# Performance work log

Measured on AMD Instinct MI355X. Metric: run time of the kernel, lower is better.

## Reference

```python
import jax, jax.numpy as jnp
import numpy as np

B, TQ, TV, D, UNITS = 16, 2048, 2048, 1024, 1024

def setup_inputs() -> dict:
    key = jax.random.key(0)
    k1, k2, k3 = jax.random.split(key, 3)
    query = jax.random.normal(k1, (B, TQ, UNITS), dtype=jnp.float32)
    values = jax.random.normal(k2, (B, TV, D), dtype=jnp.float32)
    # Glorot-ish scale for the Dense kernel
    W_kernel = jax.random.normal(k3, (D, UNITS), dtype=jnp.float32) * (1.0 / np.sqrt(D))
    W_bias = jnp.zeros((UNITS,), dtype=jnp.float32)
    return {"query": query, "values": values, "W_kernel": W_kernel, "W_bias": W_bias}

def reference(query, values, W_kernel, W_bias):
    # keys = Dense(values): [B, Tv, units]
    keys = jnp.einsum('bvd,du->bvu', values, W_kernel) + W_bias
    # score = query @ keys^T: [B, Tq, Tv]
    score = jnp.einsum('bqu,bvu->bqv', query, keys)
    alignment = jax.nn.softmax(score, axis=-1)
    # context = alignment @ values: [B, Tq, d_v]
    context = jnp.einsum('bqv,bvd->bqd', alignment, values)
    return (context, alignment)
```

## Files before the change

kernel.cpp:

```cpp
#include <hip/hip_runtime.h>
#include <hip/hip_bf16.h>


#define B_  16
#define TQ_ 2048
#define TV_ 2048
#define D_  1024
#define U_  1024

typedef __attribute__((ext_vector_type(8))) short bf16x8;
typedef __attribute__((ext_vector_type(4))) float f32x4;

__device__ __forceinline__ short f2bf(float x) {
    union { float f; unsigned u; } v; v.f = x;
    unsigned r = v.u + 0x7fffu + ((v.u >> 16) & 1u);
    return (short)(r >> 16);
}
__device__ __forceinline__ float bf2f(short h) {
    union { unsigned u; float f; } v;
    v.u = ((unsigned)(unsigned short)h) << 16;
    return v.f;
}

__device__ __forceinline__ void gld16(const short* g, short* l) {
    __builtin_amdgcn_global_load_lds(
        (const __attribute__((address_space(1))) void*)g,
        (__attribute__((address_space(3))) void*)l, 16, 0, 0);
}

#define MFMA_QUAD(MB, NB)                                                       \
    __builtin_amdgcn_s_setprio(1);                                              \
    _Pragma("unroll")                                                           \
    for (int mf = 0; mf < 4; ++mf)                                              \
        _Pragma("unroll")                                                       \
        for (int nf = 0; nf < 2; ++nf)                                          \
            _Pragma("unroll")                                                   \
            for (int ks = 0; ks < 2; ++ks)                                      \
                acc[(MB) + mf][(NB) + nf] =                                     \
                    __builtin_amdgcn_mfma_f32_16x16x32_bf16(                    \
                        afr[mf][ks], bfr[(NB) + nf][ks],                        \
                        acc[(MB) + mf][(NB) + nf], 0, 0, 0);                    \
    __builtin_amdgcn_s_setprio(0);

template<int NPLANES, int SPLIT_OUT, int KT>
__global__ __launch_bounds__(512, 2) void gemm8(
    const short* __restrict__ Ahi, const short* __restrict__ Alo,
    const short* __restrict__ Bhi, const short* __restrict__ Blo,
    float* __restrict__ C, short* __restrict__ Chi, short* __restrict__ Clo,
    int lda, int ldb, int ldc, size_t sAz, size_t sBz, size_t sCz)
{
    constexpr int NT = NPLANES * KT;
    __shared__ short sA[2][16384];
    __shared__ short sB[2][16384];

    const int tid  = threadIdx.x;
    const int lane = tid & 63, wid = tid >> 6;
    const int wm = (wid >> 2) << 7;
    const int wn = (wid & 3) << 6;
    const int l15 = lane & 15, l4 = lane >> 4, l7 = lane & 7;
    const int sr   = tid >> 3;
    const int colS = ((tid & 7) ^ (sr & 7)) << 3;
    const int wvB  = wid << 9;

    const size_t z    = blockIdx.z;
    const size_t row0 = (size_t)blockIdx.y << 8;
    const size_t col0 = (size_t)blockIdx.x << 8;
    const short* Abh = Ahi + z * sAz + row0 * (size_t)lda;
    const short* Abl = (NPLANES == 3) ? Alo + z * sAz + row0 * (size_t)lda : nullptr;
    const short* Bbh = Bhi + z * sBz + col0 * (size_t)ldb;
    const short* Bbl = (NPLANES == 3) ? Blo + z * sBz + col0 * (size_t)ldb : nullptr;

    auto aSrc = [&](int t) -> const short* {
        const int p = t / KT;
        const short* base = (NPLANES == 3 && p == 2) ? Abl : Abh;
        return base + ((t - p * KT) << 6);
    };
    auto bSrc = [&](int t) -> const short* {
        const int p = t / KT;
        const short* base = (NPLANES == 3 && p == 1) ? Bbl : Bbh;
        return base + ((t - p * KT) << 6);
    };
    auto stageA = [&](int t, int h) {
        const short* g = aSrc(t) + (size_t)((h << 7) + sr) * lda + colS;
        short* l = &sA[t & 1][(h << 13) + wvB];
        gld16(g, l);
        gld16(g + (size_t)(lda << 6), l + 4096);
    };
    auto stageB = [&](int t, int h) {
        const short* g = bSrc(t) + (size_t)((h << 7) + sr) * ldb + colS;
        short* l = &sB[t & 1][(h << 13) + wvB];
        gld16(g, l);
        gld16(g + (size_t)(ldb << 6), l + 4096);
    };

    f32x4 acc[8][4];
    #pragma unroll
    for (int i = 0; i < 8; ++i)
        #pragma unroll
        for (int j = 0; j < 4; ++j)
            acc[i][j] = (f32x4){0.f, 0.f, 0.f, 0.f};

    stageB(0, 0); stageB(0, 1); stageA(0, 0); stageA(0, 1);
    stageB(1, 0); stageB(1, 1); stageA(1, 0);
    asm volatile("s_waitcnt vmcnt(6)" ::: "memory");
    __builtin_amdgcn_s_barrier();

    #pragma unroll 1
    for (int t = 0; t < NT; ++t) {
        const short* sAb = sA[t & 1];
        const short* sBb = sB[t & 1];
        bf16x8 afr[4][2], bfr[4][2];

        #pragma unroll
        for (int nf = 0; nf < 4; ++nf)
            #pragma unroll
            for (int ks = 0; ks < 2; ++ks)
                bfr[nf][ks] = *(const bf16x8*)&sBb[((wn + (nf << 4) + l15) << 6)
                                + ((((ks << 2) | l4) ^ l7) << 3)];
        #pragma unroll
        for (int mf = 0; mf < 4; ++mf)
            #pragma unroll
            for (int ks = 0; ks < 2; ++ks)
                afr[mf][ks] = *(const bf16x8*)&sAb[((wm + (mf << 4) + l15) << 6)
                                + ((((ks << 2) | l4) ^ l7) << 3)];
        if (t + 1 < NT) stageA(t + 1, 1);
        __builtin_amdgcn_s_barrier();
        asm volatile("s_waitcnt lgkmcnt(0)" ::: "memory");
        __builtin_amdgcn_sched_barrier(0);
        MFMA_QUAD(0, 0)
        __builtin_amdgcn_s_barrier();

        if (t + 2 < NT) stageB(t + 2, 0);
        __builtin_amdgcn_s_barrier();
        MFMA_QUAD(0, 2)
        __builtin_amdgcn_s_barrier();

        #pragma unroll
        for (int mf = 0; mf < 4; ++mf)
            #pragma unroll
            for (int ks = 0; ks < 2; ++ks)
                afr[mf][ks] = *(const bf16x8*)&sAb[((wm + 64 + (mf << 4) + l15) << 6)
                                + ((((ks << 2) | l4) ^ l7) << 3)];
        if (t + 2 < NT) stageB(t + 2, 1);
        __builtin_amdgcn_s_barrier();
        asm volatile("s_waitcnt lgkmcnt(0)" ::: "memory");
        __builtin_amdgcn_sched_barrier(0);
        MFMA_QUAD(4, 2)
        __builtin_amdgcn_s_barrier();

        if (t + 2 < NT) stageA(t + 2, 0);
        __builtin_amdgcn_s_barrier();
        MFMA_QUAD(4, 0)
        if (t < NT - 2)       asm volatile("s_waitcnt vmcnt(6)" ::: "memory");
        else if (t == NT - 2) asm volatile("s_waitcnt vmcnt(0)" ::: "memory");
        __builtin_amdgcn_s_barrier();
    }

    if (SPLIT_OUT) {
        #pragma unroll
        for (int mf = 0; mf < 8; ++mf)
            #pragma unroll
            for (int nf = 0; nf < 4; ++nf)
                #pragma unroll
                for (int r = 0; r < 4; ++r) {
                    const float x = acc[mf][nf][r];
                    const short h = f2bf(x);
                    const short lo = f2bf(x - bf2f(h));
                    const size_t idx = (row0 + wm + (mf << 4) + (l4 << 2) + r) * (size_t)ldc
                                       + col0 + wn + (nf << 4) + l15;
                    Chi[idx] = h;
                    Clo[idx] = lo;
                }
    } else {
        float* Cb = C + z * sCz;
        #pragma unroll
        for (int mf = 0; mf < 8; ++mf)
            #pragma unroll
            for (int nf = 0; nf < 4; ++nf)
                #pragma unroll
                for (int r = 0; r < 4; ++r)
                    Cb[(row0 + wm + (mf << 4) + (l4 << 2) + r) * (size_t)ldc
                       + col0 + wn + (nf << 4) + l15] = acc[mf][nf][r];
    }
}

__global__ __launch_bounds__(256, 2) void gemm_ctx(
    const float* __restrict__ A, const short* __restrict__ Bt, float* __restrict__ C,
    int lda, int ldb, int ldc, int K, size_t sA, size_t sB, size_t sC)
{
    __shared__ short sA16[128 * 32], sB16[128 * 32];
    const int tid = threadIdx.x;
    const int lane = tid & 63, wave = tid >> 6;
    const int wm = (wave >> 1) << 6, wn = (wave & 1) << 6;
    const int l15 = lane & 15, l4 = lane >> 4;
    const int lr = lane >> 2, lc = (lane & 3) << 3;
    const size_t row0 = (size_t)blockIdx.y << 7, col0 = (size_t)blockIdx.x << 7;
    const float* Ab = A + (size_t)blockIdx.z * sA + row0 * (size_t)lda;
    const short* Bb = Bt + (size_t)blockIdx.z * sB + col0 * (size_t)ldb;

    f32x4 acc[4][4];
    for (int i = 0; i < 4; ++i)
        for (int j = 0; j < 4; ++j)
            acc[i][j] = (f32x4){0.f, 0.f, 0.f, 0.f};

    for (int kt = 0; kt < K; kt += 32) {
        __syncthreads();
        for (int r = 0; r < 4; ++r) {
            const int flat = (r << 8) + tid;
            const int row = flat >> 3, c = (flat & 7) << 2;
            const float4 va = *(const float4*)(Ab + (size_t)row * lda + kt + c);
            short4 h;
            h.x = f2bf(va.x); h.y = f2bf(va.y); h.z = f2bf(va.z); h.w = f2bf(va.w);
            *(short4*)&sA16[(row << 5) + c] = h;
        }
        for (int t = 0; t < 2; ++t) {
            const int rbase = (wave << 5) + (t << 4);
            gld16(Bb + (size_t)(rbase + lr) * ldb + kt + lc, &sB16[rbase << 5]);
        }
        __syncthreads();
        const int ko = l4 << 3;
        bf16x8 ah[4], bh[4];
        for (int i = 0; i < 4; ++i) {
            ah[i] = *(const bf16x8*)&sA16[((wm + (i << 4) + l15) << 5) + ko];
            bh[i] = *(const bf16x8*)&sB16[((wn + (i << 4) + l15) << 5) + ko];
        }
        for (int i = 0; i < 4; ++i)
            for (int j = 0; j < 4; ++j)
                acc[i][j] = __builtin_amdgcn_mfma_f32_16x16x32_bf16(ah[i], bh[j], acc[i][j], 0, 0, 0);
    }

    float* Cb = C + (size_t)blockIdx.z * sC;
    for (int i = 0; i < 4; ++i)
        for (int j = 0; j < 4; ++j)
            for (int r = 0; r < 4; ++r)
                Cb[(row0 + wm + (i << 4) + (l4 << 2) + r) * (size_t)ldc
                   + col0 + wn + (j << 4) + l15] = acc[i][j][r];
}

__global__ __launch_bounds__(256) void split_f32(
    const float* __restrict__ X, short* __restrict__ hi, short* __restrict__ lo)
{
    const size_t i = ((size_t)blockIdx.x * 256 + threadIdx.x) << 2;
    const float4 v = *(const float4*)(X + i);
    short4 h, l;
    h.x = f2bf(v.x); l.x = f2bf(v.x - bf2f(h.x));
    h.y = f2bf(v.y); l.y = f2bf(v.y - bf2f(h.y));
    h.z = f2bf(v.z); l.z = f2bf(v.z - bf2f(h.z));
    h.w = f2bf(v.w); l.w = f2bf(v.w - bf2f(h.w));
    *(short4*)(hi + i) = h;
    *(short4*)(lo + i) = l;
}

__global__ __launch_bounds__(256) void split_values(
    const float* __restrict__ V, short* __restrict__ Vhi,
    short* __restrict__ Vlo, short* __restrict__ Vt)
{
    __shared__ float tile[32][33];
    const int b = blockIdx.z;
    const int d0 = blockIdx.x << 5, v0 = blockIdx.y << 5;
    const float* Vb = V + (size_t)b * TV_ * D_;
    const size_t pb = (size_t)b * TV_ * D_;
    short* Vtb = Vt + (size_t)b * D_ * TV_;
    const int tx = threadIdx.x, ty = threadIdx.y;
    for (int k = 0; k < 4; ++k) {
        const int v = v0 + ty + (k << 3);
        const float x = Vb[(size_t)v * D_ + d0 + tx];
        tile[ty + (k << 3)][tx] = x;
        const short h = f2bf(x);
        Vhi[pb + (size_t)v * D_ + d0 + tx] = h;
        Vlo[pb + (size_t)v * D_ + d0 + tx] = f2bf(x - bf2f(h));
    }
    __syncthreads();
    for (int k = 0; k < 4; ++k)
        Vtb[(size_t)(d0 + ty + (k << 3)) * TV_ + v0 + tx] = f2bf(tile[tx][ty + (k << 3)]);
}

__global__ __launch_bounds__(256) void softmax_rows(
    float* __restrict__ S, short* __restrict__ A16)
{
    float* p = S + (size_t)blockIdx.x * TV_;
    const int t = threadIdx.x;
    const int lane = t & 63, wave = t >> 6;
    float4 a = *(const float4*)(p + (t << 2));
    float4 b = *(const float4*)(p + 1024 + (t << 2));
    float m = fmaxf(fmaxf(fmaxf(a.x, a.y), fmaxf(a.z, a.w)),
                    fmaxf(fmaxf(b.x, b.y), fmaxf(b.z, b.w)));
    for (int off = 32; off; off >>= 1) m = fmaxf(m, __shfl_xor(m, off, 64));
    __shared__ float redm[4], reds[4];
    if (lane == 0) redm[wave] = m;
    __syncthreads();
    m = fmaxf(fmaxf(redm[0], redm[1]), fmaxf(redm[2], redm[3]));
    a.x = __expf(a.x - m); a.y = __expf(a.y - m);
    a.z = __expf(a.z - m); a.w = __expf(a.w - m);
    b.x = __expf(b.x - m); b.y = __expf(b.y - m);
    b.z = __expf(b.z - m); b.w = __expf(b.w - m);
    float s = a.x + a.y + a.z + a.w + b.x + b.y + b.z + b.w;
    for (int off = 32; off; off >>= 1) s += __shfl_xor(s, off, 64);
    if (lane == 0) reds[wave] = s;
    __syncthreads();
    s = reds[0] + reds[1] + reds[2] + reds[3];
    const float inv = 1.0f / s;
    a.x *= inv; a.y *= inv; a.z *= inv; a.w *= inv;
    b.x *= inv; b.y *= inv; b.z *= inv; b.w *= inv;
    *(float4*)(p + (t << 2)) = a;
    *(float4*)(p + 1024 + (t << 2)) = b;
    if (A16) {
        short* q = A16 + (size_t)blockIdx.x * TV_;
        short4 ha, hb;
        ha.x = f2bf(a.x); ha.y = f2bf(a.y); ha.z = f2bf(a.z); ha.w = f2bf(a.w);
        hb.x = f2bf(b.x); hb.y = f2bf(b.y); hb.z = f2bf(b.z); hb.w = f2bf(b.w);
        *(short4*)(q + (t << 2)) = ha;
        *(short4*)(q + 1024 + (t << 2)) = hb;
    }
}

extern "C" void kernel_launch(void* const* d_in, const int* in_sizes, int n_in,
                              void* d_out, int out_size, void* d_ws, size_t ws_size,
                              hipStream_t stream)
{
    const float* query  = (const float*)d_in[0];
    const float* values = (const float*)d_in[1];
    const float* Wk     = (const float*)d_in[2];

    const size_t NQ = (size_t)B_ * TQ_ * D_;
    const size_t NV = (size_t)B_ * TV_ * D_;
    const size_t NW = (size_t)D_ * U_;
    const size_t NA = (size_t)B_ * TQ_ * TV_;

    float* context = (float*)d_out;
    float* align   = (float*)d_out + NQ;

    short* Phi = (short*)d_out;
    short* Plo = Phi + NQ;
    short* Qhi = (short*)align;
    short* Qlo = Qhi + NQ;
    short* Whi = (short*)d_ws;
    short* Wlo = Whi + NW;
    short* Vhi = Wlo + NW;
    short* Vlo = Vhi + NV;
    short* Vt  = Vlo + NV;
    const size_t WS_NEED = (2 * NW + 3 * NV + NA) * sizeof(short);
    short* A16 = (ws_size >= WS_NEED) ? (Vt + NV) : nullptr;

    split_f32<<<NQ / 1024, 256, 0, stream>>>(query, Qhi, Qlo);
    split_f32<<<NW / 1024, 256, 0, stream>>>(Wk, Whi, Wlo);
    split_values<<<dim3(D_ / 32, TV_ / 32, B_), dim3(32, 8), 0, stream>>>(
        values, Vhi, Vlo, Vt);

    gemm8<3, 1, 16><<<dim3(D_ / 256, (B_ * TQ_) / 256, 1), 512, 0, stream>>>(
        Qhi, Qlo, Whi, Wlo, nullptr, Phi, Plo, U_, U_, D_, 0, 0, 0);

    gemm8<3, 0, 16><<<dim3(TV_ / 256, TQ_ / 256, B_), 512, 0, stream>>>(
        Phi, Plo, Vhi, Vlo, align, nullptr, nullptr, D_, D_, TV_,
        (size_t)TQ_ * D_, (size_t)TV_ * D_, (size_t)TQ_ * TV_);

    softmax_rows<<<B_ * TQ_, 256, 0, stream>>>(align, A16);

    if (A16)
        gemm8<1, 0, 32><<<dim3(D_ / 256, TQ_ / 256, B_), 512, 0, stream>>>(
            A16, nullptr, Vt, nullptr, context, nullptr, nullptr, TV_, TV_, D_,
            (size_t)TQ_ * TV_, (size_t)D_ * TV_, (size_t)TQ_ * D_);
    else
        gemm_ctx<<<dim3(D_ / 128, TQ_ / 128, B_), 256, 0, stream>>>(
            align, Vt, context, TV_, TV_, D_, TV_,
            (size_t)TQ_ * TV_, (size_t)D_ * TV_, (size_t)TQ_ * D_);
}
```

Before: 1.528 ms.

## Software-pipeline LDS fragment loads with MFMA and remap workgroups across XCDs

Rewrites the GEMM main loop so LDS fragment reads for the next quarter or next K tile are issued while the current MFMA quads run. It ping-pongs two B fragment register sets, unrolls the loop by two, and reorders the global-to-LDS staging and waitcnt points. It also remaps the flat workgroup index so consecutive blocks are spread across the 8 XCDs. The aim is to hide LDS latency and drop explicit lgkmcnt stalls, at the cost of more register pressure and tighter ordering of barriers against buffer reuse.

```diff
diff --git a/kernel.cpp b/kernel.cpp
--- a/kernel.cpp
+++ b/kernel.cpp
@@ -28,19 +28,64 @@
         (__attribute__((address_space(3))) void*)l, 16, 0, 0);
 }
 
-#define MFMA_QUAD(MB, NB)                                                       \
-    __builtin_amdgcn_s_setprio(1);                                              \
-    _Pragma("unroll")                                                           \
-    for (int mf = 0; mf < 4; ++mf)                                              \
-        _Pragma("unroll")                                                       \
-        for (int nf = 0; nf < 2; ++nf)                                          \
-            _Pragma("unroll")                                                   \
-            for (int ks = 0; ks < 2; ++ks)                                      \
-                acc[(MB) + mf][(NB) + nf] =                                     \
-                    __builtin_amdgcn_mfma_f32_16x16x32_bf16(                    \
-                        afr[mf][ks], bfr[(NB) + nf][ks],                        \
-                        acc[(MB) + mf][(NB) + nf], 0, 0, 0);                    \
+#define CFENCE asm volatile("" ::: "memory")
+#define BAR()  do { CFENCE; __builtin_amdgcn_s_barrier(); CFENCE; } while (0)
+
+#define LDA_HALF(dst, sAb, half)                                            \
+    _Pragma("unroll")                                                       \
+    for (int mf = 0; mf < 4; ++mf)                                          \
+        _Pragma("unroll")                                                   \
+        for (int ks = 0; ks < 2; ++ks)                                      \
+            dst[mf][ks] = *(const bf16x8*)&(sAb)[((wm + ((half) << 6) + (mf << 4) + l15) << 6) \
+                            + ((((ks << 2) | l4) ^ l7) << 3)];
+
+#define LDB_PAIR(dst, sBb, pair)                                            \
+    _Pragma("unroll")                                                       \
+    for (int nf = 0; nf < 2; ++nf)                                          \
+        _Pragma("unroll")                                                   \
+        for (int ks = 0; ks < 2; ++ks)                                      \
+            dst[nf][ks] = *(const bf16x8*)&(sBb)[((wn + ((((pair) << 1) | nf) << 4) + l15) << 6) \
+                            + ((((ks << 2) | l4) ^ l7) << 3)];
+
+#define QUAD(MB, NB, BG)                                                    \
+    __builtin_amdgcn_s_setprio(1);                                          \
+    _Pragma("unroll")                                                       \
+    for (int mf = 0; mf < 4; ++mf)                                          \
+        _Pragma("unroll")                                                   \
+        for (int nf = 0; nf < 2; ++nf)                                      \
+            _Pragma("unroll")                                               \
+            for (int ks = 0; ks < 2; ++ks)                                  \
+                acc[(MB) + mf][(NB) + nf] = __builtin_amdgcn_mfma_f32_16x16x32_bf16( \
+                    afr[mf][ks], BG[nf][ks], acc[(MB) + mf][(NB) + nf], 0, 0, 0);    \
     __builtin_amdgcn_s_setprio(0);
+
+#define TILE(t, B01, B23)                                                   \
+    do {                                                                    \
+        const short* sAb = sA[(t) & 1];                                     \
+        const short* sBb = sB[(t) & 1];                                     \
+        LDB_PAIR(B23, sBb, 1)                                               \
+        QUAD(0, 0, B01)                                                     \
+        BAR();                                                              \
+        QUAD(0, 2, B23)                                                     \
+        LDA_HALF(afr, sAb, 1)                                               \
+        BAR();                                                              \
+        if ((t) + 2 < NT) stageB((t) + 2, 0);                               \
+        QUAD(4, 2, B23)                                                     \
+        if ((t) + 2 < NT) { asm volatile("s_waitcnt vmcnt(2)" ::: "memory"); } \
+        else              { asm volatile("s_waitcnt vmcnt(0)" ::: "memory"); } \
+        BAR();                                                              \
+        if ((t) + 2 < NT) {                                                 \
+            stageA((t) + 2, 0); stageA((t) + 2, 1); stageB((t) + 2, 1);     \
+        }                                                                   \
+        QUAD(4, 0, B01)                                                     \
+        if ((t) + 1 < NT) {                                                 \
+            const short* sAn = sA[((t) + 1) & 1];                           \
+            const short* sBn = sB[((t) + 1) & 1];                           \
+            LDA_HALF(afr, sAn, 0)                                           \
+            LDB_PAIR(B23, sBn, 0)                                           \
+        }                                                                   \
+        BAR();                                                              \
+    } while (0)
 
 template<int NPLANES, int SPLIT_OUT, int KT>
 __global__ __launch_bounds__(512, 2) void gemm8(
@@ -62,9 +107,18 @@
     const int colS = ((tid & 7) ^ (sr & 7)) << 3;
     const int wvB  = wid << 9;
 
-    const size_t z    = blockIdx.z;
-    const size_t row0 = (size_t)blockIdx.y << 8;
-    const size_t col0 = (size_t)blockIdx.x << 8;
+    const unsigned nx = gridDim.x, ny = gridDim.y;
+    const unsigned nwg = nx * ny * gridDim.z;
+    unsigned flat = blockIdx.x + nx * (blockIdx.y + ny * blockIdx.z);
+    if ((nwg & 7u) == 0u) flat = (flat & 7u) * (nwg >> 3) + (flat >> 3);
+    const unsigned bx = flat % nx;
+    const unsigned rem = flat / nx;
+    const unsigned by = rem % ny;
+    const unsigned bz = rem / ny;
+
+    const size_t z    = bz;
+    const size_t row0 = (size_t)by << 8;
+    const size_t col0 = (size_t)bx << 8;
     const short* Abh = Ahi + z * sAz + row0 * (size_t)lda;
     const short* Abl = (NPLANES == 3) ? Alo + z * sAz + row0 * (size_t)lda : nullptr;
     const short* Bbh = Bhi + z * sBz + col0 * (size_t)ldb;
@@ -100,60 +154,21 @@
         for (int j = 0; j < 4; ++j)
             acc[i][j] = (f32x4){0.f, 0.f, 0.f, 0.f};
 
+    bf16x8 afr[4][2];
+    bf16x8 bC[2][2], bD[2][2];
+
     stageB(0, 0); stageB(0, 1); stageA(0, 0); stageA(0, 1);
-    stageB(1, 0); stageB(1, 1); stageA(1, 0);
-    asm volatile("s_waitcnt vmcnt(6)" ::: "memory");
-    __builtin_amdgcn_s_barrier();
+    stageB(1, 0);
+    stageA(1, 0); stageA(1, 1); stageB(1, 1);
+    asm volatile("s_waitcnt vmcnt(8)" ::: "memory");
+    BAR();
+    LDA_HALF(afr, sA[0], 0)
+    LDB_PAIR(bC, sB[0], 0)
 
     #pragma unroll 1
-    for (int t = 0; t < NT; ++t) {
-        const short* sAb = sA[t & 1];
-        const short* sBb = sB[t & 1];
-        bf16x8 afr[4][2], bfr[4][2];
-
-        #pragma unroll
-        for (int nf = 0; nf < 4; ++nf)
-            #pragma unroll
-            for (int ks = 0; ks < 2; ++ks)
-                bfr[nf][ks] = *(const bf16x8*)&sBb[((wn + (nf << 4) + l15) << 6)
-                                + ((((ks << 2) | l4) ^ l7) << 3)];
-        #pragma unroll
-        for (int mf = 0; mf < 4; ++mf)
-            #pragma unroll
-            for (int ks = 0; ks < 2; ++ks)
-                afr[mf][ks] = *(const bf16x8*)&sAb[((wm + (mf << 4) + l15) << 6)
-                                + ((((ks << 2) | l4) ^ l7) << 3)];
-        if (t + 1 < NT) stageA(t + 1, 1);
-        __builtin_amdgcn_s_barrier();
-        asm volatile("s_waitcnt lgkmcnt(0)" ::: "memory");
-        __builtin_amdgcn_sched_barrier(0);
-        MFMA_QUAD(0, 0)
-        __builtin_amdgcn_s_barrier();
-
-        if (t + 2 < NT) stageB(t + 2, 0);
-        __builtin_amdgcn_s_barrier();
-        MFMA_QUAD(0, 2)
-        __builtin_amdgcn_s_barrier();
-
-        #pragma unroll
-        for (int mf = 0; mf < 4; ++mf)
-            #pragma unroll
-            for (int ks = 0; ks < 2; ++ks)
-                afr[mf][ks] = *(const bf16x8*)&sAb[((wm + 64 + (mf << 4) + l15) << 6)
-                                + ((((ks << 2) | l4) ^ l7) << 3)];
-        if (t + 2 < NT) stageB(t + 2, 1);
-        __builtin_amdgcn_s_barrier();
-        asm volatile("s_waitcnt lgkmcnt(0)" ::: "memory");
-        __builtin_amdgcn_sched_barrier(0);
-        MFMA_QUAD(4, 2)
-        __builtin_amdgcn_s_barrier();
-
-        if (t + 2 < NT) stageA(t + 2, 0);
-        __builtin_amdgcn_s_barrier();
-        MFMA_QUAD(4, 0)
-        if (t < NT - 2)       asm volatile("s_waitcnt vmcnt(6)" ::: "memory");
-        else if (t == NT - 2) asm volatile("s_waitcnt vmcnt(0)" ::: "memory");
-        __builtin_amdgcn_s_barrier();
+    for (int t = 0; t < NT; t += 2) {
+        TILE(t, bC, bD);
+        TILE(t + 1, bD, bC);
     }
 
     if (SPLIT_OUT) {
```

Result: faster. 1.428 ms (-6.6%).
